# Performance work log

Hardware: AMD Instinct MI355X
Metric: run time of the kernel (lower is better)

Reference implementation:

```python
import jax, jax.numpy as jnp
import numpy as np

B, L, C = 2, 2048, 1024
H = 16
D = C // H  # 64
MAX_SCALE_MUL = float(np.log(100.0))
EPS = 1e-12


def setup_inputs() -> dict:
    key = jax.random.key(0)
    ks = jax.random.split(key, 6)
    x = jax.random.normal(ks[0], (B, L, C), dtype=jnp.float32)
    attn_bias = jax.random.normal(ks[1], (1, 1, L, L), dtype=jnp.float32) * 0.02
    W_qkv = jax.random.normal(ks[2], (3 * C, C), dtype=jnp.float32) * (1.0 / np.sqrt(C))
    q_bias = jnp.zeros((C,), dtype=jnp.float32)
    v_bias = jnp.zeros((C,), dtype=jnp.float32)
    scale_mul = jnp.full((1, H, 1, 1), np.log(4.0), dtype=jnp.float32)
    W_proj = jax.random.normal(ks[3], (C, C), dtype=jnp.float32) * (1.0 / np.sqrt(C))
    b_proj = jnp.zeros((C,), dtype=jnp.float32)
    return {"x": x, "attn_bias": attn_bias, "W_qkv": W_qkv, "q_bias": q_bias,
            "v_bias": v_bias, "scale_mul": scale_mul, "W_proj": W_proj, "b_proj": b_proj}


def _l2norm(t):
    # F.normalize(dim=-1): x / max(||x||_2, eps)
    n = jnp.sqrt(jnp.sum(t * t, axis=-1, keepdims=True))
    return t / jnp.maximum(n, EPS)


def reference(x, attn_bias, W_qkv, q_bias, v_bias, scale_mul, W_proj, b_proj):
    bias = jnp.concatenate([q_bias, jnp.zeros_like(q_bias), v_bias])  # (3C,)
    qkv = x @ W_qkv.T + bias                     # (B, L, 3C)
    qkv = qkv.reshape(B, L, 3, H, D)
    q, k, v = jnp.moveaxis(qkv, 2, 0)            # each (B, L, H, D)
    q = jnp.transpose(q, (0, 2, 1, 3))           # (B, H, L, D)
    k = jnp.transpose(k, (0, 2, 1, 3))
    v = jnp.transpose(v, (0, 2, 1, 3))
    # attn_l2_norm path: scale = 1, learned per-head scale clamped at log(100)
    sm = jnp.exp(jnp.minimum(scale_mul, MAX_SCALE_MUL))  # (1, H, 1, 1)
    q = _l2norm(q) * sm
    k = _l2norm(k)
    scores = jnp.einsum('bhqd,bhkd->bhqk', q, k) + attn_bias  # scale=1
    attn = jax.nn.softmax(scores, axis=-1)
    out = jnp.einsum('bhqk,bhkd->bhqd', attn, v)  # (B, H, L, D)
    out = jnp.transpose(out, (0, 2, 1, 3)).reshape(B, L, C)
    return out @ W_proj.T + b_proj
```

## Files before the change

kernel.cpp:

```cpp
#include <hip/hip_runtime.h>


typedef __bf16 bf16x8 __attribute__((ext_vector_type(8)));
typedef __bf16 bf16x4 __attribute__((ext_vector_type(4)));
typedef float  f32x4  __attribute__((ext_vector_type(4)));

#define BB 2
#define LL 2048
#define CC 1024
#define HH 16
#define DD 64
#define LOG2E 1.44269504088896f

__device__ __forceinline__ f32x4 mfma_16x16x32(bf16x8 a, bf16x8 b, f32x4 c) {
    return __builtin_amdgcn_mfma_f32_16x16x32_bf16(a, b, c, 0, 0, 0);
}

__device__ __forceinline__ void gload_lds16(const __bf16* g, __bf16* lds) {
    __builtin_amdgcn_global_load_lds(
        (const __attribute__((address_space(1))) unsigned int*)g,
        (__attribute__((address_space(3))) unsigned int*)lds,
        16, 0, 0);
}

__device__ __forceinline__ unsigned pk_bf16(float a, float b) {
    unsigned short ua = __builtin_bit_cast(unsigned short, (__bf16)a);
    unsigned short ub = __builtin_bit_cast(unsigned short, (__bf16)b);
    return (unsigned)ua | ((unsigned)ub << 16);
}

__global__ __launch_bounds__(256) void cvt_bf16_kernel(const float* __restrict__ in,
                                                       __bf16* __restrict__ out, int n4) {
    int i = blockIdx.x * 256 + threadIdx.x;
    if (i >= n4) return;
    float4 v = reinterpret_cast<const float4*>(in)[i];
    bf16x4 o;
    o[0] = (__bf16)v.x; o[1] = (__bf16)v.y; o[2] = (__bf16)v.z; o[3] = (__bf16)v.w;
    reinterpret_cast<bf16x4*>(out)[i] = o;
}

__global__ __launch_bounds__(256) void bias_prep_kernel(const float* __restrict__ bias,
                                                        __bf16* __restrict__ bias_bf) {
    __shared__ float wmax[4];
    const int l = blockIdx.x, tid = threadIdx.x;
    const int w = tid >> 6;
    float4 a = reinterpret_cast<const float4*>(bias + (size_t)l * 2048)[tid];
    float4 b = reinterpret_cast<const float4*>(bias + (size_t)l * 2048 + 1024)[tid];
    float m = fmaxf(fmaxf(fmaxf(a.x, a.y), fmaxf(a.z, a.w)),
                    fmaxf(fmaxf(b.x, b.y), fmaxf(b.z, b.w)));
#pragma unroll
    for (int off = 1; off < 64; off <<= 1) m = fmaxf(m, __shfl_xor(m, off, 64));
    if ((tid & 63) == 0) wmax[w] = m;
    __syncthreads();
    float M = fmaxf(fmaxf(wmax[0], wmax[1]), fmaxf(wmax[2], wmax[3]));
    bf16x4 o0, o1;
    o0[0] = (__bf16)((a.x - M) * LOG2E); o0[1] = (__bf16)((a.y - M) * LOG2E);
    o0[2] = (__bf16)((a.z - M) * LOG2E); o0[3] = (__bf16)((a.w - M) * LOG2E);
    o1[0] = (__bf16)((b.x - M) * LOG2E); o1[1] = (__bf16)((b.y - M) * LOG2E);
    o1[2] = (__bf16)((b.z - M) * LOG2E); o1[3] = (__bf16)((b.w - M) * LOG2E);
    reinterpret_cast<bf16x4*>(bias_bf + (size_t)l * 2048)[tid] = o0;
    reinterpret_cast<bf16x4*>(bias_bf + (size_t)l * 2048 + 1024)[tid] = o1;
}

__global__ __launch_bounds__(256) void gemm_qkv_fused_kernel(
    const __bf16* __restrict__ A, const __bf16* __restrict__ Bm,
    const float* __restrict__ q_bias, const float* __restrict__ v_bias,
    const float* __restrict__ scale_mul,
    __bf16* __restrict__ Qw, __bf16* __restrict__ Kw, __bf16* __restrict__ Vw) {
    __shared__ __bf16 As[128 * 64];
    __shared__ __bf16 Bs[128 * 64];
    const int tid = threadIdx.x;
    const int K = 1024;
    const int nwg = gridDim.x * gridDim.y;
    const int flat = blockIdx.y * gridDim.x + blockIdx.x;
    const int wg = (flat & 7) * (nwg >> 3) + (flat >> 3);
    const int m0 = (wg % gridDim.x) * 128, n0 = (wg / gridDim.x) * 128;
    const int w  = tid >> 6, l = tid & 63;
    const int wr = (w >> 1) * 64, wc = (w & 1) * 64;
    const int lr = l & 15, lg = l >> 4;
    const int rmask = (lr & 7) << 4;
    f32x4 acc[4][4] = {};
    const int lrow = l >> 3;
    const int celem = (((l & 7) ^ lrow) << 3);

    for (int kt = 0; kt < K; kt += 64) {
        __syncthreads();
#pragma unroll
        for (int i = 0; i < 4; ++i) {
            const int row = w * 32 + i * 8;
            gload_lds16(A + (size_t)(m0 + row + lrow) * K + kt + celem, &As[row * 64]);
            gload_lds16(Bm + (size_t)(n0 + row + lrow) * K + kt + celem, &Bs[row * 64]);
        }
        asm volatile("s_waitcnt vmcnt(0)" ::: "memory");
        __syncthreads();
#pragma unroll
        for (int kk = 0; kk < 2; ++kk) {
            bf16x8 af[4], bfr[4];
#pragma unroll
            for (int m = 0; m < 4; ++m)
                af[m] = *reinterpret_cast<const bf16x8*>(
                    (char*)As + (wr + m * 16 + lr) * 128 + ((kk * 64 + lg * 16) ^ rmask));
#pragma unroll
            for (int n = 0; n < 4; ++n)
                bfr[n] = *reinterpret_cast<const bf16x8*>(
                    (char*)Bs + (wc + n * 16 + lr) * 128 + ((kk * 64 + lg * 16) ^ rmask));
#pragma unroll
            for (int m = 0; m < 4; ++m)
#pragma unroll
                for (int n = 0; n < 4; ++n)
                    acc[m][n] = mfma_16x16x32(af[m], bfr[n], acc[m][n]);
        }
    }

    const int gcbase = n0 + wc;
    const int type = gcbase >> 10;
    const int h = (gcbase & 1023) >> 6;
    float qscale = 1.0f;
    if (type == 0) qscale = __expf(fminf(scale_mul[h], 4.60517019f)) * LOG2E;
    __bf16* dst = (type == 0) ? Qw : (type == 1) ? Kw : Vw;

#pragma unroll
    for (int m = 0; m < 4; ++m) {
        if (type != 1) {
            const float* bptr = (type == 0) ? q_bias : v_bias;
#pragma unroll
            for (int n = 0; n < 4; ++n) {
                float bv = bptr[(gcbase & 1023) + n * 16 + lr];
#pragma unroll
                for (int r = 0; r < 4; ++r) acc[m][n][r] += bv;
            }
        }
        float rs[4];
        if (type < 2) {
#pragma unroll
            for (int r = 0; r < 4; ++r) {
                float ss = 0.f;
#pragma unroll
                for (int n = 0; n < 4; ++n) ss += acc[m][n][r] * acc[m][n][r];
                rs[r] = ss;
            }
#pragma unroll
            for (int off = 1; off < 16; off <<= 1)
#pragma unroll
                for (int r = 0; r < 4; ++r) rs[r] += __shfl_xor(rs[r], off, 64);
#pragma unroll
            for (int r = 0; r < 4; ++r)
                rs[r] = ((type == 0) ? qscale : 1.0f) / fmaxf(sqrtf(rs[r]), 1e-12f);
        } else {
#pragma unroll
            for (int r = 0; r < 4; ++r) rs[r] = 1.0f;
        }
        const int rowg = m0 + wr + m * 16 + lg * 4;
#pragma unroll
        for (int n = 0; n < 4; ++n) {
            const int d = n * 16 + lr;
#pragma unroll
            for (int r = 0; r < 4; ++r) {
                const int row = rowg + r;
                const int bb = row >> 11, ll = row & 2047;
                dst[((size_t)((bb << 4) + h) * 2048 + ll) * 64 + d] =
                    (__bf16)(acc[m][n][r] * rs[r]);
            }
        }
    }
}

__global__ __launch_bounds__(256) void gemm_proj_kernel(
    const __bf16* __restrict__ A, const __bf16* __restrict__ Bm,
    float* __restrict__ Cf, const float* __restrict__ bias, int M, int N, int K) {
    __shared__ __bf16 As[128 * 64];
    __shared__ __bf16 Bs[128 * 64];
    const int tid = threadIdx.x;
    const int nwg = gridDim.x * gridDim.y;
    const int flat = blockIdx.y * gridDim.x + blockIdx.x;
    const int wg = (flat & 7) * (nwg >> 3) + (flat >> 3);
    const int m0 = (wg % gridDim.x) * 128, n0 = (wg / gridDim.x) * 128;
    const int w  = tid >> 6, l = tid & 63;
    const int wr = (w >> 1) * 64, wc = (w & 1) * 64;
    const int lr = l & 15, lg = l >> 4;
    const int rmask = (lr & 7) << 4;
    f32x4 acc[4][4] = {};
    const int lrow = l >> 3;
    const int celem = (((l & 7) ^ lrow) << 3);

    for (int kt = 0; kt < K; kt += 64) {
        __syncthreads();
#pragma unroll
        for (int i = 0; i < 4; ++i) {
            const int row = w * 32 + i * 8;
            gload_lds16(A + (size_t)(m0 + row + lrow) * K + kt + celem, &As[row * 64]);
            gload_lds16(Bm + (size_t)(n0 + row + lrow) * K + kt + celem, &Bs[row * 64]);
        }
        asm volatile("s_waitcnt vmcnt(0)" ::: "memory");
        __syncthreads();
#pragma unroll
        for (int kk = 0; kk < 2; ++kk) {
            bf16x8 af[4], bfr[4];
#pragma unroll
            for (int m = 0; m < 4; ++m)
                af[m] = *reinterpret_cast<const bf16x8*>(
                    (char*)As + (wr + m * 16 + lr) * 128 + ((kk * 64 + lg * 16) ^ rmask));
#pragma unroll
            for (int n = 0; n < 4; ++n)
                bfr[n] = *reinterpret_cast<const bf16x8*>(
                    (char*)Bs + (wc + n * 16 + lr) * 128 + ((kk * 64 + lg * 16) ^ rmask));
#pragma unroll
            for (int m = 0; m < 4; ++m)
#pragma unroll
                for (int n = 0; n < 4; ++n)
                    acc[m][n] = mfma_16x16x32(af[m], bfr[n], acc[m][n]);
        }
    }
#pragma unroll
    for (int m = 0; m < 4; ++m)
#pragma unroll
        for (int n = 0; n < 4; ++n) {
            const int row = m0 + wr + m * 16 + lg * 4;
            const int col = n0 + wc + n * 16 + lr;
#pragma unroll
            for (int r = 0; r < 4; ++r)
                Cf[(size_t)(row + r) * N + col] = acc[m][n][r] + bias[col];
        }
}

__global__ __launch_bounds__(256) void v_transpose_kernel(const __bf16* __restrict__ Vin,
                                                          __bf16* __restrict__ Vt) {
    __shared__ __bf16 T[64][72];
    const int lb = blockIdx.x, bh = blockIdx.y;
    const int tid = threadIdx.x;
    const size_t base = (size_t)bh * LL * DD;
    const int row = tid >> 2, c = (tid & 3) * 16;
    {
        const __bf16* src = Vin + base + (size_t)(lb * 64 + row) * 64 + c;
        *reinterpret_cast<bf16x8*>(&T[row][c])     = *reinterpret_cast<const bf16x8*>(src);
        *reinterpret_cast<bf16x8*>(&T[row][c + 8]) = *reinterpret_cast<const bf16x8*>(src + 8);
    }
    __syncthreads();
    bf16x8 o0, o1;
#pragma unroll
    for (int j = 0; j < 8; ++j) {
        o0[j] = T[c + j][row];
        o1[j] = T[c + 8 + j][row];
    }
    __bf16* dst = Vt + base + (size_t)row * 2048 + lb * 64 + c;
    *reinterpret_cast<bf16x8*>(dst)     = o0;
    *reinterpret_cast<bf16x8*>(dst + 8) = o1;
}

__global__ __launch_bounds__(256, 4) void attn_kernel(
    const __bf16* __restrict__ Q, const __bf16* __restrict__ K,
    const __bf16* __restrict__ Vt, const __bf16* __restrict__ biasL,
    const float* __restrict__ scale_mul, __bf16* __restrict__ Octx) {
    __shared__ __bf16 KVs[2][2][64 * 64];
    const int bh = blockIdx.x, qb = blockIdx.y;
    const int tid = threadIdx.x;
    const int w = tid >> 6, l = tid & 63;
    const int lr = l & 15, lg = l >> 4;
    const int rmask = (lr & 7) << 4;
    const int b = bh >> 4, h = bh & 15;
    const size_t base = (size_t)bh * LL * DD;
    const float smh = __expf(fminf(scale_mul[h], 4.60517019f));
    const float cexp = -smh * LOG2E;

    const int gq = qb * 64 + w * 16 + lr;
    bf16x8 qf[2];
    qf[0] = *reinterpret_cast<const bf16x8*>(Q + base + (size_t)gq * 64 + lg * 8);
    qf[1] = *reinterpret_cast<const bf16x8*>(Q + base + (size_t)gq * 64 + 32 + lg * 8);
    const __bf16* brow = biasL + (size_t)gq * 2048 + lg * 4;

    const int srow = tid >> 2;
    const int scb  = (tid & 3) * 32;
    const int smask = (srow & 7) << 4;
    const __bf16* kgbase = K  + base + (size_t)srow * 64   + (tid & 3) * 16;
    const __bf16* vgbase = Vt + base + (size_t)srow * 2048 + (tid & 3) * 16;

    bf16x8 k0, k1, v0, v1;
    auto stage_regs = [&](int kb) {
        const __bf16* kg = kgbase + (size_t)kb * 64 * 64;
        k0 = *reinterpret_cast<const bf16x8*>(kg);
        k1 = *reinterpret_cast<const bf16x8*>(kg + 8);
        const __bf16* vg = vgbase + kb * 64;
        v0 = *reinterpret_cast<const bf16x8*>(vg);
        v1 = *reinterpret_cast<const bf16x8*>(vg + 8);
    };
    auto write_lds = [&](int buf) {
        char* kp = (char*)KVs[buf][0] + srow * 128;
        char* vp = (char*)KVs[buf][1] + srow * 128;
        *reinterpret_cast<bf16x8*>(kp + (scb ^ smask))        = k0;
        *reinterpret_cast<bf16x8*>(kp + ((scb + 16) ^ smask)) = k1;
        *reinterpret_cast<bf16x8*>(vp + (scb ^ smask))        = v0;
        *reinterpret_cast<bf16x8*>(vp + ((scb + 16) ^ smask)) = v1;
    };

    stage_regs(0);
    write_lds(0);

    f32x4 Oa[4] = {};
    float lsum = 0.f;
    int cur = 0;

    bf16x4 bcur[4];
#pragma unroll
    for (int t = 0; t < 4; ++t)
        bcur[t] = *reinterpret_cast<const bf16x4*>(brow + t * 16);

    for (int kb = 0; kb < 32; ++kb) {
        __syncthreads();
        if (kb < 31) stage_regs(kb + 1);

        bf16x4 bnext[4];
        if (kb < 31) {
#pragma unroll
            for (int t = 0; t < 4; ++t)
                bnext[t] = *reinterpret_cast<const bf16x4*>(brow + (kb + 1) * 64 + t * 16);
        }

        const char* Kc = (const char*)KVs[cur][0];
        const char* Vc = (const char*)KVs[cur][1];

        f32x4 sa[4];
#pragma unroll
        for (int t = 0; t < 4; ++t)
#pragma unroll
            for (int r = 0; r < 4; ++r)
                sa[t][r] = (float)bcur[t][r] + cexp;

        __builtin_amdgcn_s_setprio(1);
#pragma unroll
        for (int t = 0; t < 4; ++t) {
            const char* kr = Kc + (t * 16 + lr) * 128;
            bf16x8 kf0 = *reinterpret_cast<const bf16x8*>(kr + ((lg * 16) ^ rmask));
            bf16x8 kf1 = *reinterpret_cast<const bf16x8*>(kr + ((64 + lg * 16) ^ rmask));
            sa[t] = mfma_16x16x32(kf0, qf[0], sa[t]);
            sa[t] = mfma_16x16x32(kf1, qf[1], sa[t]);
        }
        __builtin_amdgcn_s_setprio(0);

        float p[4][4];
#pragma unroll
        for (int t = 0; t < 4; ++t)
#pragma unroll
            for (int r = 0; r < 4; ++r) {
                p[t][r] = exp2f(sa[t][r]);
                lsum += p[t][r];
            }
        union Upa { unsigned u[4]; bf16x8 v; } pa0, pa1;
        pa0.u[0] = pk_bf16(p[0][0], p[0][1]); pa0.u[1] = pk_bf16(p[0][2], p[0][3]);
        pa0.u[2] = pk_bf16(p[1][0], p[1][1]); pa0.u[3] = pk_bf16(p[1][2], p[1][3]);
        pa1.u[0] = pk_bf16(p[2][0], p[2][1]); pa1.u[1] = pk_bf16(p[2][2], p[2][3]);
        pa1.u[2] = pk_bf16(p[3][0], p[3][1]); pa1.u[3] = pk_bf16(p[3][2], p[3][3]);

        __builtin_amdgcn_s_setprio(1);
#pragma unroll
        for (int t = 0; t < 4; ++t) {
            const char* vr = Vc + (t * 16 + lr) * 128;
            union Uv { uint2 d[2]; bf16x8 v; } vf0, vf1;
            vf0.d[0] = *reinterpret_cast<const uint2*>(vr + ((lg * 8) ^ rmask));
            vf0.d[1] = *reinterpret_cast<const uint2*>(vr + ((32 + lg * 8) ^ rmask));
            vf1.d[0] = *reinterpret_cast<const uint2*>(vr + ((64 + lg * 8) ^ rmask));
            vf1.d[1] = *reinterpret_cast<const uint2*>(vr + ((96 + lg * 8) ^ rmask));
            Oa[t] = mfma_16x16x32(pa0.v, vf0.v, Oa[t]);
            Oa[t] = mfma_16x16x32(pa1.v, vf1.v, Oa[t]);
        }
        __builtin_amdgcn_s_setprio(0);

        if (kb < 31) {
            write_lds(cur ^ 1);
#pragma unroll
            for (int t = 0; t < 4; ++t) bcur[t] = bnext[t];
        }
        cur ^= 1;
    }

    lsum += __shfl_xor(lsum, 16, 64);
    lsum += __shfl_xor(lsum, 32, 64);
    float inv[4];
#pragma unroll
    for (int r = 0; r < 4; ++r) inv[r] = 1.0f / __shfl(lsum, lg * 4 + r, 64);

#pragma unroll
    for (int t = 0; t < 4; ++t)
#pragma unroll
        for (int r = 0; r < 4; ++r) {
            const int row = qb * 64 + w * 16 + lg * 4 + r;
            float o = Oa[t][r] * inv[r];
            Octx[((size_t)(b * 2048 + row)) * 1024 + h * 64 + t * 16 + lr] = (__bf16)o;
        }
}

extern "C" void kernel_launch(void* const* d_in, const int* in_sizes, int n_in,
                              void* d_out, int out_size, void* d_ws, size_t ws_size,
                              hipStream_t stream) {
    const float* x         = (const float*)d_in[0];
    const float* attn_bias = (const float*)d_in[1];
    const float* W_qkv     = (const float*)d_in[2];
    const float* q_bias    = (const float*)d_in[3];
    const float* v_bias    = (const float*)d_in[4];
    const float* scale_mul = (const float*)d_in[5];
    const float* W_proj    = (const float*)d_in[6];
    const float* b_proj    = (const float*)d_in[7];
    float* out = (float*)d_out;

    char* ws = (char*)d_ws;
    size_t off = 0;
    auto alloc = [&](size_t bytes) {
        void* p = ws + off;
        off = (off + bytes + 255) & ~(size_t)255;
        return p;
    };
    __bf16* xb      = (__bf16*)alloc((size_t)4096 * 1024 * 2);
    __bf16* wqkvb   = (__bf16*)alloc((size_t)3072 * 1024 * 2);
    __bf16* wprojb  = (__bf16*)alloc((size_t)1024 * 1024 * 2);
    __bf16* Qw      = (__bf16*)alloc((size_t)BB * HH * LL * DD * 2);
    __bf16* Kw      = (__bf16*)alloc((size_t)BB * HH * LL * DD * 2);
    __bf16* Vw      = (__bf16*)alloc((size_t)BB * HH * LL * DD * 2);
    __bf16* Oc      = (__bf16*)alloc((size_t)4096 * 1024 * 2);
    __bf16* bias_bf = (__bf16*)alloc((size_t)2048 * 2048 * 2);
    __bf16* Vt      = (__bf16*)alloc((size_t)BB * HH * LL * DD * 2);

    cvt_bf16_kernel<<<4096, 256, 0, stream>>>(x, xb, 4096 * 1024 / 4);
    cvt_bf16_kernel<<<3072, 256, 0, stream>>>(W_qkv, wqkvb, 3072 * 1024 / 4);
    cvt_bf16_kernel<<<1024, 256, 0, stream>>>(W_proj, wprojb, 1024 * 1024 / 4);

    gemm_qkv_fused_kernel<<<dim3(32, 24), 256, 0, stream>>>(
        xb, wqkvb, q_bias, v_bias, scale_mul, Qw, Kw, Vw);

    bias_prep_kernel<<<2048, 256, 0, stream>>>(attn_bias, bias_bf);
    v_transpose_kernel<<<dim3(32, 32), 256, 0, stream>>>(Vw, Vt);

    attn_kernel<<<dim3(32, 32), 256, 0, stream>>>(Qw, Kw, Vt, bias_bf, scale_mul, Oc);

    gemm_proj_kernel<<<dim3(32, 8), 256, 0, stream>>>(
        Oc, wprojb, out, b_proj, 4096, 1024, 1024);
}
```

Measured before the change: 187.1 us.

## Triple-buffer K/V tiles with direct global-to-LDS async loads

Replaces the register-staged K/V tile copy (global load to VGPRs, then ds_write) with global_load_lds direct-to-LDS transfers, using a per-lane XOR-swizzled source column so the existing LDS read swizzle still matches. The double buffer becomes a three-stage ring with prefetch two tiles ahead, synchronised by explicit vmcnt waits and one barrier per iteration. setprio hints are dropped and launch bounds drop to 3 blocks per CU to fit the larger LDS footprint. This aims to hide global latency and free the registers used for staging, at the cost of less occupancy and fragile hand-counted vmcnt values.

```diff
diff --git a/kernel.cpp b/kernel.cpp
--- a/kernel.cpp
+++ b/kernel.cpp
@@ -247,11 +247,11 @@
     *reinterpret_cast<bf16x8*>(dst + 8) = o1;
 }
 
-__global__ __launch_bounds__(256, 4) void attn_kernel(
+__global__ __launch_bounds__(256, 3) void attn_kernel(
     const __bf16* __restrict__ Q, const __bf16* __restrict__ K,
     const __bf16* __restrict__ Vt, const __bf16* __restrict__ biasL,
     const float* __restrict__ scale_mul, __bf16* __restrict__ Octx) {
-    __shared__ __bf16 KVs[2][2][64 * 64];
+    __shared__ __bf16 KVs[3][2][64 * 64];
     const int bh = blockIdx.x, qb = blockIdx.y;
     const int tid = threadIdx.x;
     const int w = tid >> 6, l = tid & 63;
@@ -268,55 +268,43 @@
     qf[1] = *reinterpret_cast<const bf16x8*>(Q + base + (size_t)gq * 64 + 32 + lg * 8);
     const __bf16* brow = biasL + (size_t)gq * 2048 + lg * 4;
 
-    const int srow = tid >> 2;
-    const int scb  = (tid & 3) * 32;
-    const int smask = (srow & 7) << 4;
-    const __bf16* kgbase = K  + base + (size_t)srow * 64   + (tid & 3) * 16;
-    const __bf16* vgbase = Vt + base + (size_t)srow * 2048 + (tid & 3) * 16;
-
-    bf16x8 k0, k1, v0, v1;
-    auto stage_regs = [&](int kb) {
-        const __bf16* kg = kgbase + (size_t)kb * 64 * 64;
-        k0 = *reinterpret_cast<const bf16x8*>(kg);
-        k1 = *reinterpret_cast<const bf16x8*>(kg + 8);
-        const __bf16* vg = vgbase + kb * 64;
-        v0 = *reinterpret_cast<const bf16x8*>(vg);
-        v1 = *reinterpret_cast<const bf16x8*>(vg + 8);
+    const int lrow = l >> 3;
+    const int celem = (((l & 7) ^ lrow) << 3);
+    auto stage = [&](int buf, int kb_) {
+        __bf16* Kd = &KVs[buf][0][0];
+        __bf16* Vd = &KVs[buf][1][0];
+#pragma unroll
+        for (int i = 0; i < 2; ++i) {
+            const int row = w * 16 + i * 8;
+            gload_lds16(K + base + ((size_t)kb_ * 64 + row + lrow) * 64 + celem, Kd + row * 64);
+            gload_lds16(Vt + base + (size_t)(row + lrow) * 2048 + kb_ * 64 + celem, Vd + row * 64);
+        }
     };
-    auto write_lds = [&](int buf) {
-        char* kp = (char*)KVs[buf][0] + srow * 128;
-        char* vp = (char*)KVs[buf][1] + srow * 128;
-        *reinterpret_cast<bf16x8*>(kp + (scb ^ smask))        = k0;
-        *reinterpret_cast<bf16x8*>(kp + ((scb + 16) ^ smask)) = k1;
-        *reinterpret_cast<bf16x8*>(vp + (scb ^ smask))        = v0;
-        *reinterpret_cast<bf16x8*>(vp + ((scb + 16) ^ smask)) = v1;
+    auto load_bias = [&](int kb_, bf16x4 (&bv)[4]) {
+#pragma unroll
+        for (int t = 0; t < 4; ++t)
+            bv[t] = *reinterpret_cast<const bf16x4*>(brow + kb_ * 64 + t * 16);
     };
-
-    stage_regs(0);
-    write_lds(0);
 
     f32x4 Oa[4] = {};
     float lsum = 0.f;
-    int cur = 0;
-
     bf16x4 bcur[4];
-#pragma unroll
-    for (int t = 0; t < 4; ++t)
-        bcur[t] = *reinterpret_cast<const bf16x4*>(brow + t * 16);
-
+
+    stage(0, 0);
+    load_bias(0, bcur);
+    stage(1, 1);
+    asm volatile("s_waitcnt vmcnt(8)" ::: "memory");
+    __builtin_amdgcn_s_barrier();
+
+#pragma unroll 1
     for (int kb = 0; kb < 32; ++kb) {
-        __syncthreads();
-        if (kb < 31) stage_regs(kb + 1);
-
         bf16x4 bnext[4];
-        if (kb < 31) {
-#pragma unroll
-            for (int t = 0; t < 4; ++t)
-                bnext[t] = *reinterpret_cast<const bf16x4*>(brow + (kb + 1) * 64 + t * 16);
-        }
-
-        const char* Kc = (const char*)KVs[cur][0];
-        const char* Vc = (const char*)KVs[cur][1];
+        if (kb < 31) load_bias(kb + 1, bnext);
+        __builtin_amdgcn_sched_barrier(0);
+        if (kb < 30) stage((kb + 2) % 3, kb + 2);
+
+        const char* Kc = (const char*)&KVs[kb % 3][0][0];
+        const char* Vc = (const char*)&KVs[kb % 3][1][0];
 
         f32x4 sa[4];
 #pragma unroll
@@ -325,7 +313,6 @@
             for (int r = 0; r < 4; ++r)
                 sa[t][r] = (float)bcur[t][r] + cexp;
 
-        __builtin_amdgcn_s_setprio(1);
 #pragma unroll
         for (int t = 0; t < 4; ++t) {
             const char* kr = Kc + (t * 16 + lr) * 128;
@@ -334,7 +321,6 @@
             sa[t] = mfma_16x16x32(kf0, qf[0], sa[t]);
             sa[t] = mfma_16x16x32(kf1, qf[1], sa[t]);
         }
-        __builtin_amdgcn_s_setprio(0);
 
         float p[4][4];
 #pragma unroll
@@ -350,7 +336,6 @@
         pa1.u[0] = pk_bf16(p[2][0], p[2][1]); pa1.u[1] = pk_bf16(p[2][2], p[2][3]);
         pa1.u[2] = pk_bf16(p[3][0], p[3][1]); pa1.u[3] = pk_bf16(p[3][2], p[3][3]);
 
-        __builtin_amdgcn_s_setprio(1);
 #pragma unroll
         for (int t = 0; t < 4; ++t) {
             const char* vr = Vc + (t * 16 + lr) * 128;
@@ -362,14 +347,14 @@
             Oa[t] = mfma_16x16x32(pa0.v, vf0.v, Oa[t]);
             Oa[t] = mfma_16x16x32(pa1.v, vf1.v, Oa[t]);
         }
-        __builtin_amdgcn_s_setprio(0);
 
         if (kb < 31) {
-            write_lds(cur ^ 1);
 #pragma unroll
             for (int t = 0; t < 4; ++t) bcur[t] = bnext[t];
-        }
-        cur ^= 1;
+            if (kb < 30) asm volatile("s_waitcnt vmcnt(8)" ::: "memory");
+            else         asm volatile("s_waitcnt vmcnt(4)" ::: "memory");
+            __builtin_amdgcn_s_barrier();
+        }
     }
 
     lsum += __shfl_xor(lsum, 16, 64);
```

Result: slower. 206.2 us (+10.2%).

## Compute softmax row sums with MFMA and keep attention bias in fp32

Applied to the files above, without the earlier changes.

The per-row softmax denominator is now computed by extra MFMAs that multiply the packed probabilities by a ones vector. This replaces the per-element VALU adds and the cross-lane shuffle reduction. The bias preprocessing now writes fp32 instead of bf16, and the attention kernel drops the constant exponent offset and the setprio hints. In exchange, the attention kernel and bias prep move twice the bias bytes, and each key block adds two MFMAs.

```diff
diff --git a/kernel.cpp b/kernel.cpp
--- a/kernel.cpp
+++ b/kernel.cpp
@@ -40,7 +40,7 @@
 }
 
 __global__ __launch_bounds__(256) void bias_prep_kernel(const float* __restrict__ bias,
-                                                        __bf16* __restrict__ bias_bf) {
+                                                        float* __restrict__ bias_f) {
     __shared__ float wmax[4];
     const int l = blockIdx.x, tid = threadIdx.x;
     const int w = tid >> 6;
@@ -53,13 +53,13 @@
     if ((tid & 63) == 0) wmax[w] = m;
     __syncthreads();
     float M = fmaxf(fmaxf(wmax[0], wmax[1]), fmaxf(wmax[2], wmax[3]));
-    bf16x4 o0, o1;
-    o0[0] = (__bf16)((a.x - M) * LOG2E); o0[1] = (__bf16)((a.y - M) * LOG2E);
-    o0[2] = (__bf16)((a.z - M) * LOG2E); o0[3] = (__bf16)((a.w - M) * LOG2E);
-    o1[0] = (__bf16)((b.x - M) * LOG2E); o1[1] = (__bf16)((b.y - M) * LOG2E);
-    o1[2] = (__bf16)((b.z - M) * LOG2E); o1[3] = (__bf16)((b.w - M) * LOG2E);
-    reinterpret_cast<bf16x4*>(bias_bf + (size_t)l * 2048)[tid] = o0;
-    reinterpret_cast<bf16x4*>(bias_bf + (size_t)l * 2048 + 1024)[tid] = o1;
+    float4 o0, o1;
+    o0.x = (a.x - M) * LOG2E; o0.y = (a.y - M) * LOG2E;
+    o0.z = (a.z - M) * LOG2E; o0.w = (a.w - M) * LOG2E;
+    o1.x = (b.x - M) * LOG2E; o1.y = (b.y - M) * LOG2E;
+    o1.z = (b.z - M) * LOG2E; o1.w = (b.w - M) * LOG2E;
+    reinterpret_cast<float4*>(bias_f + (size_t)l * 2048)[tid] = o0;
+    reinterpret_cast<float4*>(bias_f + (size_t)l * 2048 + 1024)[tid] = o1;
 }
 
 __global__ __launch_bounds__(256) void gemm_qkv_fused_kernel(
@@ -249,8 +249,8 @@
 
 __global__ __launch_bounds__(256, 4) void attn_kernel(
     const __bf16* __restrict__ Q, const __bf16* __restrict__ K,
-    const __bf16* __restrict__ Vt, const __bf16* __restrict__ biasL,
-    const float* __restrict__ scale_mul, __bf16* __restrict__ Octx) {
+    const __bf16* __restrict__ Vt, const float* __restrict__ biasF,
+    __bf16* __restrict__ Octx) {
     __shared__ __bf16 KVs[2][2][64 * 64];
     const int bh = blockIdx.x, qb = blockIdx.y;
     const int tid = threadIdx.x;
@@ -259,14 +259,16 @@
     const int rmask = (lr & 7) << 4;
     const int b = bh >> 4, h = bh & 15;
     const size_t base = (size_t)bh * LL * DD;
-    const float smh = __expf(fminf(scale_mul[h], 4.60517019f));
-    const float cexp = -smh * LOG2E;
 
     const int gq = qb * 64 + w * 16 + lr;
     bf16x8 qf[2];
     qf[0] = *reinterpret_cast<const bf16x8*>(Q + base + (size_t)gq * 64 + lg * 8);
     qf[1] = *reinterpret_cast<const bf16x8*>(Q + base + (size_t)gq * 64 + 32 + lg * 8);
-    const __bf16* brow = biasL + (size_t)gq * 2048 + lg * 4;
+    const float* brow = biasF + (size_t)gq * 2048 + lg * 4;
+
+    bf16x8 ones;
+#pragma unroll
+    for (int j = 0; j < 8; ++j) ones[j] = (__bf16)1.0f;
 
     const int srow = tid >> 2;
     const int scb  = (tid & 3) * 32;
@@ -296,23 +298,23 @@
     write_lds(0);
 
     f32x4 Oa[4] = {};
-    float lsum = 0.f;
+    f32x4 ls = {};
     int cur = 0;
 
-    bf16x4 bcur[4];
+    f32x4 bcur[4];
 #pragma unroll
     for (int t = 0; t < 4; ++t)
-        bcur[t] = *reinterpret_cast<const bf16x4*>(brow + t * 16);
+        bcur[t] = *reinterpret_cast<const f32x4*>(brow + t * 16);
 
     for (int kb = 0; kb < 32; ++kb) {
         __syncthreads();
         if (kb < 31) stage_regs(kb + 1);
 
-        bf16x4 bnext[4];
+        f32x4 bnext[4];
         if (kb < 31) {
 #pragma unroll
             for (int t = 0; t < 4; ++t)
-                bnext[t] = *reinterpret_cast<const bf16x4*>(brow + (kb + 1) * 64 + t * 16);
+                bnext[t] = *reinterpret_cast<const f32x4*>(brow + (kb + 1) * 64 + t * 16);
         }
 
         const char* Kc = (const char*)KVs[cur][0];
@@ -320,12 +322,7 @@
 
         f32x4 sa[4];
 #pragma unroll
-        for (int t = 0; t < 4; ++t)
-#pragma unroll
-            for (int r = 0; r < 4; ++r)
-                sa[t][r] = (float)bcur[t][r] + cexp;
-
-        __builtin_amdgcn_s_setprio(1);
+        for (int t = 0; t < 4; ++t) sa[t] = bcur[t];
 #pragma unroll
         for (int t = 0; t < 4; ++t) {
             const char* kr = Kc + (t * 16 + lr) * 128;
@@ -334,23 +331,22 @@
             sa[t] = mfma_16x16x32(kf0, qf[0], sa[t]);
             sa[t] = mfma_16x16x32(kf1, qf[1], sa[t]);
         }
-        __builtin_amdgcn_s_setprio(0);
 
         float p[4][4];
 #pragma unroll
         for (int t = 0; t < 4; ++t)
 #pragma unroll
-            for (int r = 0; r < 4; ++r) {
+            for (int r = 0; r < 4; ++r)
                 p[t][r] = exp2f(sa[t][r]);
-                lsum += p[t][r];
-            }
         union Upa { unsigned u[4]; bf16x8 v; } pa0, pa1;
         pa0.u[0] = pk_bf16(p[0][0], p[0][1]); pa0.u[1] = pk_bf16(p[0][2], p[0][3]);
         pa0.u[2] = pk_bf16(p[1][0], p[1][1]); pa0.u[3] = pk_bf16(p[1][2], p[1][3]);
         pa1.u[0] = pk_bf16(p[2][0], p[2][1]); pa1.u[1] = pk_bf16(p[2][2], p[2][3]);
         pa1.u[2] = pk_bf16(p[3][0], p[3][1]); pa1.u[3] = pk_bf16(p[3][2], p[3][3]);
 
-        __builtin_amdgcn_s_setprio(1);
+        ls = mfma_16x16x32(pa0.v, ones, ls);
+        ls = mfma_16x16x32(pa1.v, ones, ls);
+
 #pragma unroll
         for (int t = 0; t < 4; ++t) {
             const char* vr = Vc + (t * 16 + lr) * 128;
@@ -362,7 +358,6 @@
             Oa[t] = mfma_16x16x32(pa0.v, vf0.v, Oa[t]);
             Oa[t] = mfma_16x16x32(pa1.v, vf1.v, Oa[t]);
         }
-        __builtin_amdgcn_s_setprio(0);
 
         if (kb < 31) {
             write_lds(cur ^ 1);
@@ -372,11 +367,9 @@
         cur ^= 1;
     }
 
-    lsum += __shfl_xor(lsum, 16, 64);
-    lsum += __shfl_xor(lsum, 32, 64);
     float inv[4];
 #pragma unroll
-    for (int r = 0; r < 4; ++r) inv[r] = 1.0f / __shfl(lsum, lg * 4 + r, 64);
+    for (int r = 0; r < 4; ++r) inv[r] = 1.0f / ls[r];
 
 #pragma unroll
     for (int t = 0; t < 4; ++t)
@@ -415,7 +408,7 @@
     __bf16* Kw      = (__bf16*)alloc((size_t)BB * HH * LL * DD * 2);
     __bf16* Vw      = (__bf16*)alloc((size_t)BB * HH * LL * DD * 2);
     __bf16* Oc      = (__bf16*)alloc((size_t)4096 * 1024 * 2);
-    __bf16* bias_bf = (__bf16*)alloc((size_t)2048 * 2048 * 2);
+    float*  bias_f  = (float*)alloc((size_t)2048 * 2048 * 4);
     __bf16* Vt      = (__bf16*)alloc((size_t)BB * HH * LL * DD * 2);
 
     cvt_bf16_kernel<<<4096, 256, 0, stream>>>(x, xb, 4096 * 1024 / 4);
@@ -425,10 +418,10 @@
     gemm_qkv_fused_kernel<<<dim3(32, 24), 256, 0, stream>>>(
         xb, wqkvb, q_bias, v_bias, scale_mul, Qw, Kw, Vw);
 
-    bias_prep_kernel<<<2048, 256, 0, stream>>>(attn_bias, bias_bf);
+    bias_prep_kernel<<<2048, 256, 0, stream>>>(attn_bias, bias_f);
     v_transpose_kernel<<<dim3(32, 32), 256, 0, stream>>>(Vw, Vt);
 
-    attn_kernel<<<dim3(32, 32), 256, 0, stream>>>(Qw, Kw, Vt, bias_bf, scale_mul, Oc);
+    attn_kernel<<<dim3(32, 32), 256, 0, stream>>>(Qw, Kw, Vt, bias_f, Oc);
 
     gemm_proj_kernel<<<dim3(32, 8), 256, 0, stream>>>(
         Oc, wprojb, out, b_proj, 4096, 1024, 1024);
```

Result: no change. 186.7 us (-0.2%).

## Split attention over key halves with fp32 partials and a combine kernel

Applied to the files above, without the earlier changes.

The attention kernel now splits the key range into two halves across blockIdx.z and uses 512-thread blocks covering 128 query rows. Each half writes unnormalized fp32 partial outputs and row sums, and a new combine kernel adds them, normalizes and converts to bf16. Row sums are now computed with an MFMA against a ones vector. V is written in a permuted layout so each fragment is one 16-byte LDS read. The constant exponent offset and the s_setprio hints are dropped. This buys more parallelism and cheaper LDS reads, at the cost of roughly 32 MB of extra fp32 partial traffic, one more kernel launch, and workspace aliasing of Of0 over earlier buffers.

```diff
diff --git a/kernel.cpp b/kernel.cpp
--- a/kernel.cpp
+++ b/kernel.cpp
@@ -224,7 +224,7 @@
 }
 
 __global__ __launch_bounds__(256) void v_transpose_kernel(const __bf16* __restrict__ Vin,
-                                                          __bf16* __restrict__ Vt) {
+                                                          __bf16* __restrict__ Vp) {
     __shared__ __bf16 T[64][72];
     const int lb = blockIdx.x, bh = blockIdx.y;
     const int tid = threadIdx.x;
@@ -236,83 +236,80 @@
         *reinterpret_cast<bf16x8*>(&T[row][c + 8]) = *reinterpret_cast<const bf16x8*>(src + 8);
     }
     __syncthreads();
-    bf16x8 o0, o1;
-#pragma unroll
-    for (int j = 0; j < 8; ++j) {
-        o0[j] = T[c + j][row];
-        o1[j] = T[c + 8 + j][row];
-    }
-    __bf16* dst = Vt + base + (size_t)row * 2048 + lb * 64 + c;
-    *reinterpret_cast<bf16x8*>(dst)     = o0;
-    *reinterpret_cast<bf16x8*>(dst + 8) = o1;
-}
-
-__global__ __launch_bounds__(256, 4) void attn_kernel(
+    __bf16 val[16];
+#pragma unroll
+    for (int jj = 0; jj < 16; ++jj) {
+        const int cp = c + jj;
+        const int wb = cp & 31;
+        const int kloc = (cp & ~31) | (((wb >> 3) & 3) << 2) | (((wb >> 2) & 1) << 4) | (wb & 3);
+        val[jj] = T[kloc][row];
+    }
+    __bf16* dst = Vp + base + (size_t)row * 2048 + lb * 64 + c;
+    *reinterpret_cast<bf16x8*>(dst)     = *reinterpret_cast<bf16x8*>(&val[0]);
+    *reinterpret_cast<bf16x8*>(dst + 8) = *reinterpret_cast<bf16x8*>(&val[8]);
+}
+
+__global__ __launch_bounds__(512, 6) void attn_kernel(
     const __bf16* __restrict__ Q, const __bf16* __restrict__ K,
-    const __bf16* __restrict__ Vt, const __bf16* __restrict__ biasL,
-    const float* __restrict__ scale_mul, __bf16* __restrict__ Octx) {
+    const __bf16* __restrict__ Vp, const __bf16* __restrict__ biasB,
+    float* __restrict__ Of0, float* __restrict__ Of1, float* __restrict__ lsF) {
     __shared__ __bf16 KVs[2][2][64 * 64];
-    const int bh = blockIdx.x, qb = blockIdx.y;
+    const int bh = blockIdx.x, qb = blockIdx.y, sp = blockIdx.z;
     const int tid = threadIdx.x;
     const int w = tid >> 6, l = tid & 63;
     const int lr = l & 15, lg = l >> 4;
     const int rmask = (lr & 7) << 4;
     const int b = bh >> 4, h = bh & 15;
     const size_t base = (size_t)bh * LL * DD;
-    const float smh = __expf(fminf(scale_mul[h], 4.60517019f));
-    const float cexp = -smh * LOG2E;
-
-    const int gq = qb * 64 + w * 16 + lr;
+    const int kb0 = sp * 16;
+
+    const int gq = qb * 128 + w * 16 + lr;
     bf16x8 qf[2];
     qf[0] = *reinterpret_cast<const bf16x8*>(Q + base + (size_t)gq * 64 + lg * 8);
     qf[1] = *reinterpret_cast<const bf16x8*>(Q + base + (size_t)gq * 64 + 32 + lg * 8);
-    const __bf16* brow = biasL + (size_t)gq * 2048 + lg * 4;
-
-    const int srow = tid >> 2;
-    const int scb  = (tid & 3) * 32;
+    const __bf16* brow = biasB + (size_t)gq * 2048 + lg * 4;
+
+    bf16x8 ones;
+#pragma unroll
+    for (int j = 0; j < 8; ++j) ones[j] = (__bf16)1.0f;
+
+    const int srow = w * 8 + (l >> 3);
+    const int sce  = (l & 7) * 8;
     const int smask = (srow & 7) << 4;
-    const __bf16* kgbase = K  + base + (size_t)srow * 64   + (tid & 3) * 16;
-    const __bf16* vgbase = Vt + base + (size_t)srow * 2048 + (tid & 3) * 16;
-
-    bf16x8 k0, k1, v0, v1;
+    const __bf16* kgbase = K  + base + (size_t)srow * 64   + sce;
+    const __bf16* vgbase = Vp + base + (size_t)srow * 2048 + sce;
+
+    bf16x8 k0, v0;
     auto stage_regs = [&](int kb) {
-        const __bf16* kg = kgbase + (size_t)kb * 64 * 64;
-        k0 = *reinterpret_cast<const bf16x8*>(kg);
-        k1 = *reinterpret_cast<const bf16x8*>(kg + 8);
-        const __bf16* vg = vgbase + kb * 64;
-        v0 = *reinterpret_cast<const bf16x8*>(vg);
-        v1 = *reinterpret_cast<const bf16x8*>(vg + 8);
+        k0 = *reinterpret_cast<const bf16x8*>(kgbase + (size_t)kb * 64 * 64);
+        v0 = *reinterpret_cast<const bf16x8*>(vgbase + kb * 64);
     };
     auto write_lds = [&](int buf) {
-        char* kp = (char*)KVs[buf][0] + srow * 128;
-        char* vp = (char*)KVs[buf][1] + srow * 128;
-        *reinterpret_cast<bf16x8*>(kp + (scb ^ smask))        = k0;
-        *reinterpret_cast<bf16x8*>(kp + ((scb + 16) ^ smask)) = k1;
-        *reinterpret_cast<bf16x8*>(vp + (scb ^ smask))        = v0;
-        *reinterpret_cast<bf16x8*>(vp + ((scb + 16) ^ smask)) = v1;
+        *reinterpret_cast<bf16x8*>((char*)KVs[buf][0] + srow * 128 + ((sce * 2) ^ smask)) = k0;
+        *reinterpret_cast<bf16x8*>((char*)KVs[buf][1] + srow * 128 + ((sce * 2) ^ smask)) = v0;
     };
 
-    stage_regs(0);
+    stage_regs(kb0);
     write_lds(0);
 
     f32x4 Oa[4] = {};
-    float lsum = 0.f;
+    f32x4 ls = {};
     int cur = 0;
 
     bf16x4 bcur[4];
 #pragma unroll
     for (int t = 0; t < 4; ++t)
-        bcur[t] = *reinterpret_cast<const bf16x4*>(brow + t * 16);
-
-    for (int kb = 0; kb < 32; ++kb) {
+        bcur[t] = *reinterpret_cast<const bf16x4*>(brow + kb0 * 64 + t * 16);
+
+    for (int kb = 0; kb < 16; ++kb) {
         __syncthreads();
-        if (kb < 31) stage_regs(kb + 1);
+        if (kb < 15) stage_regs(kb0 + kb + 1);
 
         bf16x4 bnext[4];
-        if (kb < 31) {
+        if (kb < 15) {
 #pragma unroll
             for (int t = 0; t < 4; ++t)
-                bnext[t] = *reinterpret_cast<const bf16x4*>(brow + (kb + 1) * 64 + t * 16);
+                bnext[t] = *reinterpret_cast<const bf16x4*>(brow + (kb0 + kb + 1) * 64 + t * 16);
         }
 
         const char* Kc = (const char*)KVs[cur][0];
@@ -323,9 +320,8 @@
         for (int t = 0; t < 4; ++t)
 #pragma unroll
             for (int r = 0; r < 4; ++r)
-                sa[t][r] = (float)bcur[t][r] + cexp;
-
-        __builtin_amdgcn_s_setprio(1);
+                sa[t][r] = (float)bcur[t][r];
+
 #pragma unroll
         for (int t = 0; t < 4; ++t) {
             const char* kr = Kc + (t * 16 + lr) * 128;
@@ -334,37 +330,32 @@
             sa[t] = mfma_16x16x32(kf0, qf[0], sa[t]);
             sa[t] = mfma_16x16x32(kf1, qf[1], sa[t]);
         }
-        __builtin_amdgcn_s_setprio(0);
 
         float p[4][4];
 #pragma unroll
         for (int t = 0; t < 4; ++t)
 #pragma unroll
-            for (int r = 0; r < 4; ++r) {
+            for (int r = 0; r < 4; ++r)
                 p[t][r] = exp2f(sa[t][r]);
-                lsum += p[t][r];
-            }
         union Upa { unsigned u[4]; bf16x8 v; } pa0, pa1;
         pa0.u[0] = pk_bf16(p[0][0], p[0][1]); pa0.u[1] = pk_bf16(p[0][2], p[0][3]);
         pa0.u[2] = pk_bf16(p[1][0], p[1][1]); pa0.u[3] = pk_bf16(p[1][2], p[1][3]);
         pa1.u[0] = pk_bf16(p[2][0], p[2][1]); pa1.u[1] = pk_bf16(p[2][2], p[2][3]);
         pa1.u[2] = pk_bf16(p[3][0], p[3][1]); pa1.u[3] = pk_bf16(p[3][2], p[3][3]);
 
-        __builtin_amdgcn_s_setprio(1);
+        ls = mfma_16x16x32(pa0.v, ones, ls);
+        ls = mfma_16x16x32(pa1.v, ones, ls);
+
 #pragma unroll
         for (int t = 0; t < 4; ++t) {
             const char* vr = Vc + (t * 16 + lr) * 128;
-            union Uv { uint2 d[2]; bf16x8 v; } vf0, vf1;
-            vf0.d[0] = *reinterpret_cast<const uint2*>(vr + ((lg * 8) ^ rmask));
-            vf0.d[1] = *reinterpret_cast<const uint2*>(vr + ((32 + lg * 8) ^ rmask));
-            vf1.d[0] = *reinterpret_cast<const uint2*>(vr + ((64 + lg * 8) ^ rmask));
-            vf1.d[1] = *reinterpret_cast<const uint2*>(vr + ((96 + lg * 8) ^ rmask));
-            Oa[t] = mfma_16x16x32(pa0.v, vf0.v, Oa[t]);
-            Oa[t] = mfma_16x16x32(pa1.v, vf1.v, Oa[t]);
-        }
-        __builtin_amdgcn_s_setprio(0);
-
-        if (kb < 31) {
+            bf16x8 vf0 = *reinterpret_cast<const bf16x8*>(vr + ((lg * 16) ^ rmask));
+            bf16x8 vf1 = *reinterpret_cast<const bf16x8*>(vr + ((64 + lg * 16) ^ rmask));
+            Oa[t] = mfma_16x16x32(pa0.v, vf0, Oa[t]);
+            Oa[t] = mfma_16x16x32(pa1.v, vf1, Oa[t]);
+        }
+
+        if (kb < 15) {
             write_lds(cur ^ 1);
 #pragma unroll
             for (int t = 0; t < 4; ++t) bcur[t] = bnext[t];
@@ -372,20 +363,42 @@
         cur ^= 1;
     }
 
-    lsum += __shfl_xor(lsum, 16, 64);
-    lsum += __shfl_xor(lsum, 32, 64);
-    float inv[4];
-#pragma unroll
-    for (int r = 0; r < 4; ++r) inv[r] = 1.0f / __shfl(lsum, lg * 4 + r, 64);
-
+    float* Ofp = sp ? Of1 : Of0;
 #pragma unroll
     for (int t = 0; t < 4; ++t)
 #pragma unroll
         for (int r = 0; r < 4; ++r) {
-            const int row = qb * 64 + w * 16 + lg * 4 + r;
-            float o = Oa[t][r] * inv[r];
-            Octx[((size_t)(b * 2048 + row)) * 1024 + h * 64 + t * 16 + lr] = (__bf16)o;
-        }
+            const int row = qb * 128 + w * 16 + lg * 4 + r;
+            Ofp[((size_t)(b * 2048 + row)) * 1024 + h * 64 + t * 16 + lr] = Oa[t][r];
+        }
+    if (lr == 0) {
+#pragma unroll
+        for (int r = 0; r < 4; ++r) {
+            const int row = qb * 128 + w * 16 + lg * 4 + r;
+            lsF[((size_t)sp * 32 + bh) * 2048 + row] = ls[r];
+        }
+    }
+}
+
+__global__ __launch_bounds__(256) void combine_kernel(
+    const float* __restrict__ Of0, const float* __restrict__ Of1,
+    const float* __restrict__ lsF, __bf16* __restrict__ Oc) {
+    const int i = blockIdx.x * 256 + threadIdx.x;
+    const int e = i * 4;
+    const int row = e >> 10;
+    const int col = e & 1023;
+    const int h = col >> 6;
+    const int b = row >> 11, l = row & 2047;
+    const size_t lsi = ((size_t)(b * 16 + h)) * 2048 + l;
+    const float inv = 1.0f / (lsF[lsi] + lsF[(size_t)32 * 2048 + lsi]);
+    float4 a = reinterpret_cast<const float4*>(Of0)[i];
+    float4 c = reinterpret_cast<const float4*>(Of1)[i];
+    bf16x4 o;
+    o[0] = (__bf16)((a.x + c.x) * inv);
+    o[1] = (__bf16)((a.y + c.y) * inv);
+    o[2] = (__bf16)((a.z + c.z) * inv);
+    o[3] = (__bf16)((a.w + c.w) * inv);
+    reinterpret_cast<bf16x4*>(Oc)[i] = o;
 }
 
 extern "C" void kernel_launch(void* const* d_in, const int* in_sizes, int n_in,
@@ -408,15 +421,18 @@
         off = (off + bytes + 255) & ~(size_t)255;
         return p;
     };
+    __bf16* Vw      = (__bf16*)alloc((size_t)BB * HH * LL * DD * 2);
     __bf16* xb      = (__bf16*)alloc((size_t)4096 * 1024 * 2);
     __bf16* wqkvb   = (__bf16*)alloc((size_t)3072 * 1024 * 2);
     __bf16* wprojb  = (__bf16*)alloc((size_t)1024 * 1024 * 2);
     __bf16* Qw      = (__bf16*)alloc((size_t)BB * HH * LL * DD * 2);
     __bf16* Kw      = (__bf16*)alloc((size_t)BB * HH * LL * DD * 2);
-    __bf16* Vw      = (__bf16*)alloc((size_t)BB * HH * LL * DD * 2);
     __bf16* Oc      = (__bf16*)alloc((size_t)4096 * 1024 * 2);
-    __bf16* bias_bf = (__bf16*)alloc((size_t)2048 * 2048 * 2);
-    __bf16* Vt      = (__bf16*)alloc((size_t)BB * HH * LL * DD * 2);
+    __bf16* biasB   = (__bf16*)alloc((size_t)2048 * 2048 * 2);
+    __bf16* Vp      = (__bf16*)alloc((size_t)BB * HH * LL * DD * 2);
+    float*  Of1     = (float*)alloc((size_t)4096 * 1024 * 4);
+    float*  lsF     = (float*)alloc((size_t)2 * 32 * 2048 * 4);
+    float*  Of0     = (float*)d_ws;
 
     cvt_bf16_kernel<<<4096, 256, 0, stream>>>(x, xb, 4096 * 1024 / 4);
     cvt_bf16_kernel<<<3072, 256, 0, stream>>>(W_qkv, wqkvb, 3072 * 1024 / 4);
@@ -425,10 +441,12 @@
     gemm_qkv_fused_kernel<<<dim3(32, 24), 256, 0, stream>>>(
         xb, wqkvb, q_bias, v_bias, scale_mul, Qw, Kw, Vw);
 
-    bias_prep_kernel<<<2048, 256, 0, stream>>>(attn_bias, bias_bf);
-    v_transpose_kernel<<<dim3(32, 32), 256, 0, stream>>>(Vw, Vt);
-
-    attn_kernel<<<dim3(32, 32), 256, 0, stream>>>(Qw, Kw, Vt, bias_bf, scale_mul, Oc);
+    bias_prep_kernel<<<2048, 256, 0, stream>>>(attn_bias, biasB);
+    v_transpose_kernel<<<dim3(32, 32), 256, 0, stream>>>(Vw, Vp);
+
+    attn_kernel<<<dim3(32, 16, 2), 512, 0, stream>>>(Qw, Kw, Vp, biasB, Of0, Of1, lsF);
+
+    combine_kernel<<<4096, 256, 0, stream>>>(Of0, Of1, lsF, Oc);
 
     gemm_proj_kernel<<<dim3(32, 8), 256, 0, stream>>>(
         Oc, wprojb, out, b_proj, 4096, 1024, 1024);
```

Result: no change. 185.1 us (-1.1%).
